# Performance work log

Measured on AMD Instinct MI355X. Metric: run time of the kernel, lower is better.

Reference implementation:

```python
import jax, jax.numpy as jnp
import numpy as np

N_NODES = 100000
N_EDGES = 1600000
EMB = 128
N_LAYER = 5
X_DIM = 178
E_DIM = 18
BN_EPS = 1e-5


def setup_inputs() -> dict:
    key = jax.random.key(0)
    ks = jax.random.split(key, 20)
    s = 0.05  # weight scale
    inp = {}
    inp["x"] = jax.random.normal(ks[0], (N_NODES, X_DIM), jnp.float32)
    inp["edge_attr"] = jax.random.uniform(ks[1], (N_EDGES, E_DIM), jnp.float32)
    # input MLP (178 -> emb -> emb, LeakyReLU 0.1)
    inp["iw1"] = jax.random.normal(ks[2], (X_DIM, EMB), jnp.float32) * s
    inp["ib1"] = jax.random.normal(ks[3], (EMB,), jnp.float32) * s
    inp["iw2"] = jax.random.normal(ks[4], (EMB, EMB), jnp.float32) * s
    inp["ib2"] = jax.random.normal(ks[5], (EMB,), jnp.float32) * s
    # per-layer edge embedding MLP (18 -> emb -> emb, LeakyReLU 0.1)
    inp["ew1"] = jax.random.normal(ks[6], (N_LAYER, E_DIM, EMB), jnp.float32) * s
    inp["eb1"] = jax.random.normal(ks[7], (N_LAYER, EMB), jnp.float32) * s
    inp["ew2"] = jax.random.normal(ks[8], (N_LAYER, EMB, EMB), jnp.float32) * s
    inp["eb2"] = jax.random.normal(ks[9], (N_LAYER, EMB), jnp.float32) * s
    # per-layer GIN update MLP (emb -> 2emb -> emb, ReLU)
    inp["mw1"] = jax.random.normal(ks[10], (N_LAYER, EMB, 2 * EMB), jnp.float32) * s
    inp["mb1"] = jax.random.normal(ks[11], (N_LAYER, 2 * EMB), jnp.float32) * s
    inp["mw2"] = jax.random.normal(ks[12], (N_LAYER, 2 * EMB, EMB), jnp.float32) * s
    inp["mb2"] = jax.random.normal(ks[13], (N_LAYER, EMB), jnp.float32) * s
    # per-layer BatchNorm affine params
    inp["gamma"] = jnp.ones((N_LAYER, EMB), jnp.float32)
    inp["beta"] = jnp.zeros((N_LAYER, EMB), jnp.float32)
    inp["edge_index"] = jax.random.randint(ks[14], (2, N_EDGES), 0, N_NODES)
    return inp


def _leaky(v):
    return jnp.where(v > 0, v, 0.1 * v)


def reference(x, edge_attr, iw1, ib1, iw2, ib2, ew1, eb1, ew2, eb2,
              mw1, mb1, mw2, mb2, gamma, beta, edge_index):
    src = edge_index[0]  # x_j gathered from source nodes (PyG source_to_target)
    dst = edge_index[1]
    n = x.shape[0]

    # input node MLP with LeakyReLU(0.1)
    h = _leaky(x @ iw1 + ib1) @ iw2 + ib2  # [N, EMB]

    for l in range(N_LAYER):
        # edge embeddings for real edges: [E, EMB]
        ee = _leaky(edge_attr @ ew1[l] + eb1[l]) @ ew2[l] + eb2[l]
        # self-loop edges have zero edge_attr -> constant embedding vector [EMB]
        self_e = _leaky(eb1[l]) @ ew2[l] + eb2[l]
        # message = x_j + edge_emb; aggregate (add) at destination, plus self-loop term
        msg = h[src] + ee
        aggr = jax.ops.segment_sum(msg, dst, num_segments=n) + h + self_e
        # GIN update MLP (ReLU)
        hh = jnp.maximum(aggr @ mw1[l] + mb1[l], 0.0) @ mw2[l] + mb2[l]
        # BatchNorm1d (training mode: batch stats, biased variance)
        mean = hh.mean(axis=0)
        var = hh.var(axis=0)
        hh = (hh - mean) / jnp.sqrt(var + BN_EPS) * gamma[l] + beta[l]
        if l < N_LAYER - 1:
            hh = jnp.maximum(hh, 0.0)  # ReLU on all but last layer; dropout p=0 is a no-op
        h = hh

    return h  # JK == 'last'
```

## Files before the change

kernel.cpp:

```cpp
#include <hip/hip_runtime.h>
#include <hip/hip_bf16.h>
#include <hip/hip_fp16.h>
#include <cstdint>
#include <cstddef>

#define NNODES 100000
#define NEDGES 1600000
#define EMBD 128
#define NLAYER 5
#define XDIM 178
#define EDIM 18
#define BNEPS 1e-5f

typedef __attribute__((ext_vector_type(8))) short short8;
typedef __attribute__((ext_vector_type(8))) unsigned short ushort8;
typedef __attribute__((ext_vector_type(4))) float f32x4;

static __device__ __forceinline__ float leakyf(float v){ return v > 0.f ? v : 0.1f*v; }
static __device__ __forceinline__ unsigned short f2b(float v){
  __hip_bfloat16 b = __float2bfloat16(v);
  return *reinterpret_cast<unsigned short*>(&b);
}
static __device__ __forceinline__ float b2f(unsigned short u){
  __hip_bfloat16 b = *reinterpret_cast<__hip_bfloat16*>(&u);
  return __bfloat162float(b);
}
static __device__ __forceinline__ unsigned short f2h(float v){
  __half h = __float2half(v);
  return *reinterpret_cast<unsigned short*>(&h);
}
static __device__ __forceinline__ float h2f(unsigned short u){
  __half h = *reinterpret_cast<__half*>(&u);
  return __half2float(h);
}

__global__ __launch_bounds__(256) void k_hist(const int* __restrict__ dst, int* __restrict__ cnt){
  int e = blockIdx.x*256 + threadIdx.x;
  if (e < NEDGES) atomicAdd(&cnt[dst[e]], 1);
}

__global__ __launch_bounds__(256) void k_scan1(const int* __restrict__ cnt, int* __restrict__ rowptr,
                                               int* __restrict__ bsum){
  __shared__ int s[256];
  int t = threadIdx.x, i = blockIdx.x*256 + t;
  int v = (i < NNODES) ? cnt[i] : 0;
  s[t] = v; __syncthreads();
  for (int off=1; off<256; off<<=1){
    int x = (t>=off) ? s[t-off] : 0; __syncthreads();
    s[t] += x; __syncthreads();
  }
  if (i < NNODES) rowptr[i+1] = s[t];
  if (t == 255) bsum[blockIdx.x] = s[t];
}

__global__ __launch_bounds__(512) void k_scan2(const int* __restrict__ bsum, int* __restrict__ boff, int nb){
  __shared__ int s[512];
  int t = threadIdx.x;
  int v = (t < nb) ? bsum[t] : 0;
  s[t] = v; __syncthreads();
  for (int off=1; off<512; off<<=1){
    int x = (t>=off) ? s[t-off] : 0; __syncthreads();
    s[t] += x; __syncthreads();
  }
  if (t < nb) boff[t] = s[t] - v;
}

__global__ __launch_bounds__(256) void k_scan3(int* __restrict__ rowptr, const int* __restrict__ boff){
  int i = blockIdx.x*256 + threadIdx.x;
  if (i < NNODES) rowptr[i+1] += boff[i>>8];
  if (i == 0) rowptr[0] = 0;
}

__global__ __launch_bounds__(256) void k_curcopy(const int* __restrict__ rowptr, int* __restrict__ cursor){
  int i = blockIdx.x*256 + threadIdx.x;
  if (i < NNODES) cursor[i] = rowptr[i];
}

__global__ __launch_bounds__(256) void k_fill_pos(const int* __restrict__ dst, int* __restrict__ cursor,
                                                  int* __restrict__ einv){
  int e = blockIdx.x*256 + threadIdx.x;
  if (e >= NEDGES) return;
  int pos = atomicAdd(&cursor[dst[e]], 1);
  einv[pos] = e;
}

__global__ __launch_bounds__(256) void k_fill_ea(const int* __restrict__ einv, const int* __restrict__ src,
                                                 const float* __restrict__ ea,
                                                 int* __restrict__ srcp, unsigned short* __restrict__ eap24){
  int pos = blockIdx.x*256 + threadIdx.x;
  if (pos >= NEDGES) return;
  int e = einv[pos];
  srcp[pos] = src[e];
  const float* a = ea + (size_t)e*EDIM;
  float v[18];
  #pragma unroll
  for (int k=0;k<9;++k){
    float2 t = *(const float2*)(a + 2*k);
    v[2*k] = t.x; v[2*k+1] = t.y;
  }
  ushort8 r0, r1, r2;
  #pragma unroll
  for (int k=0;k<8;++k) r0[k] = f2b(v[k]);
  #pragma unroll
  for (int k=0;k<8;++k) r1[k] = f2b(v[8+k]);
  #pragma unroll
  for (int k=0;k<8;++k) r2[k] = 0;
  r2[0] = f2b(v[16]); r2[1] = f2b(v[17]);
  r2[2] = 0x3F80;
  unsigned short* o = eap24 + (size_t)pos*24;
  *reinterpret_cast<ushort8*>(o)      = r0;
  *reinterpret_cast<ushort8*>(o + 8)  = r1;
  *reinterpret_cast<ushort8*>(o + 16) = r2;
}

__global__ __launch_bounds__(256) void k_fill(const int* __restrict__ src, const int* __restrict__ dst,
                                              const float* __restrict__ ea, int* __restrict__ cursor,
                                              int* __restrict__ perm, int* __restrict__ srcp,
                                              float* __restrict__ eap){
  int e = blockIdx.x*256 + threadIdx.x;
  if (e >= NEDGES) return;
  int pos = atomicAdd(&cursor[dst[e]], 1);
  perm[pos] = e;
  srcp[pos] = src[e];
  if (eap){
    const float* a = ea + (size_t)e*EDIM;
    float* o = eap + (size_t)pos*EDIM;
    #pragma unroll
    for (int k=0;k<EDIM;++k) o[k] = a[k];
  }
}

__global__ __launch_bounds__(128) void k_selfe(const float* __restrict__ eb1, const float* __restrict__ ew2,
                                               const float* __restrict__ eb2, float* __restrict__ selfe){
  int l = blockIdx.x, c = threadIdx.x;
  const float* b1 = eb1 + l*EMBD;
  const float* w2 = ew2 + (size_t)l*EMBD*EMBD;
  float acc = eb2[l*EMBD + c];
  for (int j=0;j<EMBD;++j) acc += leakyf(b1[j]) * w2[j*EMBD + c];
  selfe[l*EMBD + c] = acc;
}

__global__ __launch_bounds__(256) void k_wc(const float* __restrict__ ew2, const float* __restrict__ mw1,
                                            float* __restrict__ wc){
  int idx = blockIdx.x*256 + threadIdx.x;
  int l = idx >> 15, rem = idx & 32767;
  int i = rem >> 8, n = rem & 255;
  const float* e = ew2 + (size_t)l*EMBD*EMBD + i*EMBD;
  const float* m = mw1 + (size_t)l*EMBD*2*EMBD + n;
  float acc = 0.f;
  #pragma unroll 4
  for (int j=0;j<EMBD;++j) acc += e[j]*m[(size_t)j*2*EMBD];
  wc[idx] = acc;
}

__global__ __launch_bounds__(256) void k_pack(const float* __restrict__ s1, int rows1,
                                              const float* __restrict__ s2, int Kreal,
                                              int Kpad, int N, __hip_bfloat16* __restrict__ out){
  int idx = blockIdx.x*256 + threadIdx.x;
  if (idx >= Kpad*N) return;
  int k = idx / N, n = idx - k*N;
  float v = 0.f;
  if (k < rows1) v = s1[(size_t)k*N + n];
  else if (k < Kreal) v = s2[(size_t)(k-rows1)*N + n];
  unsigned short hi = f2b(v);
  unsigned short lo = f2b(v - b2f(hi));
  size_t o = (size_t)(k>>5)*N*32 + (size_t)n*32 + (k&31);
  unsigned short* po = (unsigned short*)out;
  po[o] = hi;
  po[(size_t)Kpad*N + o] = lo;
}

__global__ __launch_bounds__(256) void k_s1all(
    const int* __restrict__ rowptr, const unsigned short* __restrict__ eap24,
    const float* __restrict__ ew1, const float* __restrict__ eb1,
    unsigned short* __restrict__ S1all)
{
  __shared__ __align__(16) unsigned short wlds[NLAYER*3*EMBD*8];
  int tid = threadIdx.x;
  for (int i = tid; i < NLAYER*3*EMBD*8; i += 256){
    int j = i & 7;
    int col = (i >> 3) & 127;
    int kb3 = (i >> 10) % 3;
    int l = i / 3072;
    int k = kb3*8 + j;
    float v = 0.f;
    if (k < EDIM) v = ew1[(size_t)l*EDIM*EMBD + k*EMBD + col];
    else if (k == EDIM) v = eb1[l*EMBD + col];
    wlds[i] = f2b(v);
  }
  __syncthreads();

  int lane = tid & 63;
  int lr = lane & 15, kb = lane >> 4;

  int wid = blockIdx.x*4 + (tid>>6);
  const int NW = gridDim.x*4;
  for (int node = wid; node < NNODES; node += NW){
    int rs = rowptr[node], re = rowptr[node+1];
    float s[NLAYER][8];
    #pragma unroll
    for (int l=0;l<NLAYER;++l)
      #pragma unroll
      for (int nf=0;nf<8;++nf) s[l][nf] = 0.f;

    for (int c0 = rs; c0 < re; c0 += 16){
      int cnt = re - c0;
      int idx = c0 + lr; if (idx > re-1) idx = re-1;
      short8 af = (short8)0;
      if (kb < 3){
        ushort8 t = *reinterpret_cast<const ushort8*>(eap24 + (size_t)idx*24 + kb*8);
        af = *reinterpret_cast<short8*>(&t);
      }
      if (lr >= cnt) af = (short8)0;

      #pragma unroll
      for (int l=0;l<NLAYER;++l){
        #pragma unroll
        for (int nf=0;nf<8;++nf){
          short8 bh = (short8)0;
          if (kb < 3)
            bh = *reinterpret_cast<const short8*>(&wlds[(((l*3+kb)*128) + nf*16 + lr)*8]);
          f32x4 acc = (f32x4)0.f;
          acc = __builtin_amdgcn_mfma_f32_16x16x32_bf16(af, bh, acc, 0,0,0);
          #pragma unroll
          for (int j=0;j<4;++j){
            float v = acc[j];
            s[l][nf] = fmaf(0.55f, v, s[l][nf]);
            s[l][nf] = fmaf(0.45f, fabsf(v), s[l][nf]);
          }
        }
      }
    }

    #pragma unroll
    for (int l=0;l<NLAYER;++l){
      float r[8];
      #pragma unroll
      for (int nf=0;nf<8;++nf){
        float v = s[l][nf];
        v += __shfl_xor(v, 16);
        v += __shfl_xor(v, 32);
        r[nf] = v;
      }
      float va = r[0], vb = r[1];
      if (kb == 1){ va = r[2]; vb = r[3]; }
      if (kb == 2){ va = r[4]; vb = r[5]; }
      if (kb == 3){ va = r[6]; vb = r[7]; }
      unsigned short* dst = S1all + ((size_t)l*NNODES + node)*EMBD;
      dst[kb*32 + lr]      = f2h(va);
      dst[kb*32 + 16 + lr] = f2h(vb);
    }
  }
}

__global__ __launch_bounds__(256) void k_gather_h(
    const unsigned short* __restrict__ hh,
    const int* __restrict__ rowptr, const int* __restrict__ srcp,
    const float* __restrict__ eb2l, const float* __restrict__ selfel,
    float* __restrict__ base)
{
  int tid = threadIdx.x;
  int li = tid & 31;
  int c4 = li*4;
  float4 sf4 = *(const float4*)(selfel + c4);
  float4 e24 = *(const float4*)(eb2l + c4);
  int slot = blockIdx.x*8 + (tid>>5);
  const int NS = gridDim.x*8;
  for (int node = slot; node < NNODES; node += NS){
    int rs = rowptr[node], re = rowptr[node+1];
    f32x4 b = (f32x4)0.f;
    for (int c0 = rs; c0 < re; c0 += 8){
      int cnt = re - c0;
      #pragma unroll
      for (int p=0;p<8;++p){
        int e = c0 + p; if (e > re-1) e = re-1;
        float m = (p < cnt) ? 1.f : 0.f;
        int sp = srcp[e];
        uint2 hv = *(const uint2*)(hh + (size_t)sp*EMBD + c4);
        b[0] = fmaf(m, h2f((unsigned short)(hv.x & 0xffffu)), b[0]);
        b[1] = fmaf(m, h2f((unsigned short)(hv.x >> 16)),     b[1]);
        b[2] = fmaf(m, h2f((unsigned short)(hv.y & 0xffffu)), b[2]);
        b[3] = fmaf(m, h2f((unsigned short)(hv.y >> 16)),     b[3]);
      }
    }
    float deg = (float)(re - rs);
    uint2 hn = *(const uint2*)(hh + (size_t)node*EMBD + c4);
    float4 o;
    o.x = b[0] + h2f((unsigned short)(hn.x & 0xffffu)) + sf4.x + deg*e24.x;
    o.y = b[1] + h2f((unsigned short)(hn.x >> 16))     + sf4.y + deg*e24.y;
    o.z = b[2] + h2f((unsigned short)(hn.y & 0xffffu)) + sf4.z + deg*e24.z;
    o.w = b[3] + h2f((unsigned short)(hn.y >> 16))     + sf4.w + deg*e24.w;
    *(float4*)(base + (size_t)node*EMBD + c4) = o;
  }
}

__global__ __launch_bounds__(256) void k_edge2(
    const unsigned short* __restrict__ hh, const int* __restrict__ rowptr,
    const int* __restrict__ srcp, const unsigned short* __restrict__ eap24,
    const float* __restrict__ ew1l, const float* __restrict__ eb1l,
    const float* __restrict__ eb2l, const float* __restrict__ selfel,
    float* __restrict__ S1, float* __restrict__ base, int GG)
{
  int tid = threadIdx.x;
  if ((int)blockIdx.x < GG){
    int li = tid & 31;
    int c4 = li*4;
    float4 sf4 = *(const float4*)(selfel + c4);
    float4 e24 = *(const float4*)(eb2l + c4);
    int slot = blockIdx.x*8 + (tid>>5);
    const int NS = GG*8;
    for (int node = slot; node < NNODES; node += NS){
      int rs = rowptr[node], re = rowptr[node+1];
      f32x4 b = (f32x4)0.f;
      for (int c0 = rs; c0 < re; c0 += 8){
        int cnt = re - c0;
        #pragma unroll
        for (int p=0;p<8;++p){
          int e = c0 + p; if (e > re-1) e = re-1;
          float m = (p < cnt) ? 1.f : 0.f;
          int sp = srcp[e];
          uint2 hv = *(const uint2*)(hh + (size_t)sp*EMBD + c4);
          b[0] = fmaf(m, h2f((unsigned short)(hv.x & 0xffffu)), b[0]);
          b[1] = fmaf(m, h2f((unsigned short)(hv.x >> 16)),     b[1]);
          b[2] = fmaf(m, h2f((unsigned short)(hv.y & 0xffffu)), b[2]);
          b[3] = fmaf(m, h2f((unsigned short)(hv.y >> 16)),     b[3]);
        }
      }
      float deg = (float)(re - rs);
      uint2 hn = *(const uint2*)(hh + (size_t)node*EMBD + c4);
      float4 o;
      o.x = b[0] + h2f((unsigned short)(hn.x & 0xffffu)) + sf4.x + deg*e24.x;
      o.y = b[1] + h2f((unsigned short)(hn.x >> 16))     + sf4.y + deg*e24.y;
      o.z = b[2] + h2f((unsigned short)(hn.y & 0xffffu)) + sf4.z + deg*e24.z;
      o.w = b[3] + h2f((unsigned short)(hn.y >> 16))     + sf4.w + deg*e24.w;
      *(float4*)(base + (size_t)node*EMBD + c4) = o;
    }
  } else {
    int lane = tid & 63;
    int lr = lane & 15, kb = lane >> 4;
    short8 bh[8];
    #pragma unroll
    for (int nf=0; nf<8; ++nf){
      int col = nf*16 + lr;
      ushort8 hh8;
      #pragma unroll
      for (int j=0;j<8;++j){
        int k = kb*8 + j;
        float v = 0.f;
        if (k < EDIM) v = ew1l[k*EMBD + col];
        else if (k == EDIM) v = eb1l[col];
        hh8[j] = f2b(v);
      }
      bh[nf] = *reinterpret_cast<short8*>(&hh8);
    }
    auto loadC = [&](int c0, int re)->short8{
      int cnt = re - c0;
      int idx = c0 + lr; if (idx > re-1) idx = re-1;
      short8 af = (short8)0;
      if (kb < 3){
        ushort8 t = *reinterpret_cast<const ushort8*>(eap24 + (size_t)idx*24 + kb*8);
        af = *reinterpret_cast<short8*>(&t);
      }
      if (lr >= cnt) af = (short8)0;
      return af;
    };
    const int GS = gridDim.x - GG;
    int wid = (blockIdx.x - GG)*4 + (tid>>6);
    const int NW = GS*4;
    for (int nA = wid; nA < NNODES; nA += 2*NW){
      int nB = nA + NW;
      bool hasB = (nB < NNODES);
      int rsA = rowptr[nA], reA = rowptr[nA+1];
      int rsB = 0, reB = 0;
      if (hasB){ rsB = rowptr[nB]; reB = rowptr[nB+1]; }
      float sA[8], sB[8];
      #pragma unroll
      for (int nf=0;nf<8;++nf){ sA[nf]=0.f; sB[nf]=0.f; }
      int cA = rsA, cB = rsB;
      while (cA < reA || cB < reB){
        bool dA = cA < reA, dB = cB < reB;
        short8 afA = (short8)0, afB = (short8)0;
        if (dA) afA = loadC(cA, reA);
        if (dB) afB = loadC(cB, reB);
        if (dA){
          #pragma unroll
          for (int nf=0;nf<8;++nf){
            f32x4 acc = (f32x4)0.f;
            acc = __builtin_amdgcn_mfma_f32_16x16x32_bf16(afA, bh[nf], acc, 0,0,0);
            #pragma unroll
            for (int j=0;j<4;++j){
              float v = acc[j];
              sA[nf] = fmaf(0.55f, v, sA[nf]);
              sA[nf] = fmaf(0.45f, fabsf(v), sA[nf]);
            }
          }
        }
        if (dB){
          #pragma unroll
          for (int nf=0;nf<8;++nf){
            f32x4 acc = (f32x4)0.f;
            acc = __builtin_amdgcn_mfma_f32_16x16x32_bf16(afB, bh[nf], acc, 0,0,0);
            #pragma unroll
            for (int j=0;j<4;++j){
              float v = acc[j];
              sB[nf] = fmaf(0.55f, v, sB[nf]);
              sB[nf] = fmaf(0.45f, fabsf(v), sB[nf]);
            }
          }
        }
        cA += 16; cB += 16;
      }
      {
        #pragma unroll
        for (int nf=0;nf<8;++nf){
          float v = sA[nf];
          v += __shfl_xor(v, 16);
          v += __shfl_xor(v, 32);
          sA[nf] = v;
        }
        float va = sA[0], vb = sA[1];
        if (kb == 1){ va = sA[2]; vb = sA[3]; }
        if (kb == 2){ va = sA[4]; vb = sA[5]; }
        if (kb == 3){ va = sA[6]; vb = sA[7]; }
        S1[(size_t)nA*EMBD + kb*32 + lr]      = va;
        S1[(size_t)nA*EMBD + kb*32 + 16 + lr] = vb;
      }
      if (hasB){
        #pragma unroll
        for (int nf=0;nf<8;++nf){
          float v = sB[nf];
          v += __shfl_xor(v, 16);
          v += __shfl_xor(v, 32);
          sB[nf] = v;
        }
        float va = sB[0], vb = sB[1];
        if (kb == 1){ va = sB[2]; vb = sB[3]; }
        if (kb == 2){ va = sB[4]; vb = sB[5]; }
        if (kb == 3){ va = sB[6]; vb = sB[7]; }
        S1[(size_t)nB*EMBD + kb*32 + lr]      = va;
        S1[(size_t)nB*EMBD + kb*32 + 16 + lr] = vb;
      }
    }
  }
}

__global__ __launch_bounds__(256) void k_edge(
    const float* __restrict__ h, const int* __restrict__ rowptr,
    const int* __restrict__ perm, const int* __restrict__ srcp,
    const float* __restrict__ edge_attr, const float* __restrict__ eaperm,
    const float* __restrict__ ew1l, const float* __restrict__ eb1l,
    const float* __restrict__ eb2l, const float* __restrict__ selfel,
    float* __restrict__ S1, float* __restrict__ base)
{
  __shared__ float w1s[EDIM*EMBD];
  __shared__ float b1s[EMBD];
  int tid = threadIdx.x;
  for (int i = tid; i < EDIM*EMBD; i += 256) w1s[i] = ew1l[i];
  if (tid < EMBD) b1s[tid] = eb1l[tid];
  __syncthreads();
  int lane = tid & 63;
  int node = blockIdx.x*4 + (tid >> 6);
  if (node >= NNODES) return;
  int rs = rowptr[node], re = rowptr[node+1];
  int c0 = lane*2;
  float s1x=0.f, s1y=0.f, bx=0.f, by=0.f;
  for (int i = rs; i < re; ++i){
    int s = __builtin_amdgcn_readfirstlane(srcp[i]);
    const float* ea;
    if (eaperm){
      ea = eaperm + (size_t)__builtin_amdgcn_readfirstlane(i)*EDIM;
    } else {
      ea = edge_attr + (size_t)__builtin_amdgcn_readfirstlane(perm[i])*EDIM;
    }
    float2 hs = *(const float2*)(h + (size_t)s*EMBD + c0);
    bx += hs.x; by += hs.y;
    float d0 = b1s[c0], d1 = b1s[c0+1];
    #pragma unroll
    for (int k=0;k<EDIM;++k){
      float av = ea[k];
      d0 += av * w1s[k*EMBD + c0];
      d1 += av * w1s[k*EMBD + c0 + 1];
    }
    s1x += leakyf(d0); s1y += leakyf(d1);
  }
  float deg = (float)(re - rs);
  float2 hv = *(const float2*)(h + (size_t)node*EMBD + c0);
  *(float2*)(S1 + (size_t)node*EMBD + c0) = make_float2(s1x, s1y);
  float bvx = bx + hv.x + selfel[c0]   + deg*eb2l[c0];
  float bvy = by + hv.y + selfel[c0+1] + deg*eb2l[c0+1];
  *(float2*)(base + (size_t)node*EMBD + c0) = make_float2(bvx, bvy);
}

template<int BN, int WGM, int WGN, bool ALO, bool BLO, int ACT, bool STATS, bool OBF16,
         bool CONCAT, bool KCHK, bool ABF16, bool AH16>
__global__ __launch_bounds__(512) void k_mgemm(
    const float* __restrict__ Af, const float* __restrict__ A1,
    const __hip_bfloat16* __restrict__ Ab, const unsigned short* __restrict__ Afh,
    int M, int Kreal, int Kpad, int lda,
    const __hip_bfloat16* __restrict__ Bp,
    const float* __restrict__ bias,
    float* __restrict__ Cf, __hip_bfloat16* __restrict__ Cb, int ldc,
    float* __restrict__ stats, unsigned short* __restrict__ Ch)
{
  static_assert(WGM*WGN == 8, "8 waves");
  constexpr int BM = 128;
  constexpr int MF = BM/(16*WGM);
  constexpr int NF = BN/(16*WGN);
  constexpr int LDS_ROW = 40;
  __shared__ __align__(16) unsigned short Ah[BM*LDS_ROW];
  __shared__ __align__(16) unsigned short Al[ALO ? BM*LDS_ROW : 8];
  __shared__ float ssum[STATS ? BN : 4];
  __shared__ float ssq [STATS ? BN : 4];

  int tid = threadIdx.x;
  int row0 = blockIdx.x*BM;
  int w = tid >> 6, lane = tid & 63;
  int wm = w / WGN, wn = w % WGN;
  int lr = lane & 15, kb = lane >> 4;
  int wrow = wm*MF*16, wcol = wn*NF*16;

  if (STATS && tid < BN){ ssum[tid] = 0.f; ssq[tid] = 0.f; }

  f32x4 acc[MF][NF];
  #pragma unroll
  for (int a=0;a<MF;++a)
    #pragma unroll
    for (int b=0;b<NF;++b) acc[a][b] = (f32x4)0.f;

  const size_t planeSz = (size_t)Kpad*BN;
  int sr = tid >> 2;
  int skq = (tid & 3)*8;
  int grow = row0 + sr;
  const int KS = Kpad >> 5;

  for (int ks = 0; ks < KS; ++ks){
    int k0 = ks << 5;
    int kg = k0 + skq;
    ushort8 hv, lv;
    if (ABF16){
      short8 raw = (short8)0;
      if (grow < M) raw = *reinterpret_cast<const short8*>((const unsigned short*)Ab + (size_t)grow*lda + kg);
      hv = *reinterpret_cast<ushort8*>(&raw);
    } else {
      float v[8];
      if (AH16 && (!CONCAT || kg < EMBD)){
        ushort8 raw = (ushort8)0;
        if (grow < M) raw = *reinterpret_cast<const ushort8*>(Afh + (size_t)grow*(CONCAT ? EMBD : lda) + kg);
        #pragma unroll
        for (int i=0;i<8;++i) v[i] = h2f(raw[i]);
      } else if (KCHK){
        #pragma unroll
        for (int i=0;i<8;++i)
          v[i] = (grow < M && kg+i < Kreal) ? Af[(size_t)grow*lda + kg + i] : 0.f;
      } else {
        const float* s;
        if (CONCAT) s = A1 + (size_t)grow*lda + (kg - (AH16 ? EMBD : 0));
        else        s = Af + (size_t)grow*lda + kg;
        if (CONCAT && !AH16 && kg < EMBD) s = Af + (size_t)grow*lda + kg;
        float4 p0 = make_float4(0,0,0,0), p1 = make_float4(0,0,0,0);
        if (grow < M){ p0 = *(const float4*)s; p1 = *(const float4*)(s+4); }
        v[0]=p0.x; v[1]=p0.y; v[2]=p0.z; v[3]=p0.w;
        v[4]=p1.x; v[5]=p1.y; v[6]=p1.z; v[7]=p1.w;
      }
      #pragma unroll
      for (int i=0;i<8;++i){
        unsigned short h16 = f2b(v[i]);
        hv[i] = h16;
        if (ALO) lv[i] = f2b(v[i] - b2f(h16));
      }
    }
    __syncthreads();
    *reinterpret_cast<ushort8*>(&Ah[sr*LDS_ROW + skq]) = hv;
    if (ALO && !ABF16) *reinterpret_cast<ushort8*>(&Al[sr*LDS_ROW + skq]) = lv;
    __syncthreads();

    short8 ah[MF], al[MF];
    #pragma unroll
    for (int mf=0; mf<MF; ++mf){
      int r = (wrow + mf*16 + lr)*LDS_ROW + kb*8;
      ah[mf] = *reinterpret_cast<const short8*>(&Ah[r]);
      if (ALO) al[mf] = *reinterpret_cast<const short8*>(&Al[r]);
    }
    const unsigned short* bb = (const unsigned short*)Bp + (size_t)ks*BN*32;
    short8 bh[NF], blv[NF];
    #pragma unroll
    for (int nf=0; nf<NF; ++nf){
      size_t off = (size_t)(wcol + nf*16 + lr)*32 + kb*8;
      bh[nf] = *reinterpret_cast<const short8*>(bb + off);
      if (BLO) blv[nf] = *reinterpret_cast<const short8*>(bb + planeSz + off);
    }
    #pragma unroll
    for (int mf=0; mf<MF; ++mf){
      #pragma unroll
      for (int nf=0; nf<NF; ++nf){
        acc[mf][nf] = __builtin_amdgcn_mfma_f32_16x16x32_bf16(ah[mf], bh[nf], acc[mf][nf], 0, 0, 0);
        if (BLO)
          acc[mf][nf] = __builtin_amdgcn_mfma_f32_16x16x32_bf16(ah[mf], blv[nf], acc[mf][nf], 0, 0, 0);
        if (ALO)
          acc[mf][nf] = __builtin_amdgcn_mfma_f32_16x16x32_bf16(al[mf], bh[nf], acc[mf][nf], 0, 0, 0);
      }
    }
  }

  float bcol[NF];
  #pragma unroll
  for (int nf=0; nf<NF; ++nf) bcol[nf] = bias ? bias[wcol + nf*16 + lr] : 0.f;
  float s[NF], sq[NF];
  #pragma unroll
  for (int nf=0; nf<NF; ++nf){ s[nf]=0.f; sq[nf]=0.f; }

  #pragma unroll
  for (int mf=0; mf<MF; ++mf){
    #pragma unroll
    for (int j=0; j<4; ++j){
      int r = row0 + wrow + mf*16 + kb*4 + j;
      if (r < M){
        #pragma unroll
        for (int nf=0; nf<NF; ++nf){
          int c = wcol + nf*16 + lr;
          float v = acc[mf][nf][j] + bcol[nf];
          if (ACT == 1) v = leakyf(v);
          if (ACT == 2) v = fmaxf(v, 0.f);
          if (OBF16) Cb[(size_t)r*ldc + c] = __float2bfloat16(v);
          else if (Cf) Cf[(size_t)r*ldc + c] = v;
          if (Ch) Ch[(size_t)r*ldc + c] = f2h(v);
          if (STATS){ s[nf] += v; sq[nf] += v*v; }
        }
      }
    }
  }
  if (STATS){
    #pragma unroll
    for (int nf=0; nf<NF; ++nf){
      atomicAdd(&ssum[wcol + nf*16 + lr], s[nf]);
      atomicAdd(&ssq [wcol + nf*16 + lr], sq[nf]);
    }
    __syncthreads();
    if (tid < BN){
      atomicAdd(&stats[tid], ssum[tid]);
      atomicAdd(&stats[BN + tid], ssq[tid]);
    }
  }
}

__global__ __launch_bounds__(256) void k_bn(const float* __restrict__ hh, const float* __restrict__ stats,
                                            const float* __restrict__ gamma, const float* __restrict__ beta,
                                            float* __restrict__ out, unsigned short* __restrict__ outh,
                                            int dorelu){
  int idx = blockIdx.x*256 + threadIdx.x;
  if (idx >= NNODES*(EMBD/4)) return;
  int c0 = (idx & (EMBD/4 - 1)) * 4;
  float4 v = *(const float4*)(hh + (size_t)idx*4);
  float o[4] = {v.x, v.y, v.z, v.w};
  const float invN = 1.f / (float)NNODES;
  #pragma unroll
  for (int i=0;i<4;++i){
    int c = c0 + i;
    float mean = stats[c] * invN;
    float var  = stats[EMBD + c] * invN - mean*mean;
    float inv  = rsqrtf(fmaxf(var, 0.f) + BNEPS);
    float y = (o[i] - mean) * inv * gamma[c] + beta[c];
    if (dorelu) y = fmaxf(y, 0.f);
    o[i] = y;
  }
  if (out) *(float4*)(out + (size_t)idx*4) = make_float4(o[0],o[1],o[2],o[3]);
  if (outh){
    uint2 pk;
    pk.x = (unsigned)f2h(o[0]) | ((unsigned)f2h(o[1]) << 16);
    pk.y = (unsigned)f2h(o[2]) | ((unsigned)f2h(o[3]) << 16);
    *reinterpret_cast<uint2*>(outh + (size_t)idx*4) = pk;
  }
}

extern "C" void kernel_launch(void* const* d_in, const int* in_sizes, int n_in,
                              void* d_out, int out_size, void* d_ws, size_t ws_size,
                              hipStream_t stream)
{
  const float* x   = (const float*)d_in[0];
  const float* ea  = (const float*)d_in[1];
  const float* iw1 = (const float*)d_in[2];
  const float* ib1 = (const float*)d_in[3];
  const float* iw2 = (const float*)d_in[4];
  const float* ib2 = (const float*)d_in[5];
  const float* ew1 = (const float*)d_in[6];
  const float* eb1 = (const float*)d_in[7];
  const float* ew2 = (const float*)d_in[8];
  const float* eb2 = (const float*)d_in[9];
  const float* mw1 = (const float*)d_in[10];
  const float* mb1 = (const float*)d_in[11];
  const float* mw2 = (const float*)d_in[12];
  const float* mb2 = (const float*)d_in[13];
  const float* gamma = (const float*)d_in[14];
  const float* beta  = (const float*)d_in[15];
  const int* eidx = (const int*)d_in[16];
  const int* srcI = eidx;
  const int* dstI = eidx + NEDGES;

  char* p = (char*)d_ws;
  auto alloc = [&](size_t bytes)->char*{
    char* r = p; p += (bytes + 255) & ~(size_t)255; return r;
  };
  float* S1    = (float*)alloc((size_t)NNODES*EMBD*4);
  float* base  = (float*)alloc((size_t)NNODES*EMBD*4);
  __hip_bfloat16* tbuf = (__hip_bfloat16*)alloc((size_t)NNODES*2*EMBD*2);
  int* perm   = (int*)alloc((size_t)NEDGES*4);
  int* srcp   = (int*)alloc((size_t)NEDGES*4);
  int* rowptr = (int*)alloc((size_t)(NNODES+1)*4);
  int* cursor = (int*)alloc((size_t)NNODES*4);
  int* bsum   = (int*)alloc(4096);
  int* boff   = (int*)alloc(4096);
  float* selfe = (float*)alloc(NLAYER*EMBD*4);
  float* stats = (float*)alloc(2*EMBD*4);
  float* wc    = (float*)alloc((size_t)NLAYER*EMBD*2*EMBD*4);
  __hip_bfloat16* Bi1 = (__hip_bfloat16*)alloc((size_t)192*EMBD*2*2);
  __hip_bfloat16* Bi2 = (__hip_bfloat16*)alloc((size_t)EMBD*EMBD*2*2);
  __hip_bfloat16* B1  = (__hip_bfloat16*)alloc((size_t)NLAYER*256*256*2*2);
  __hip_bfloat16* B2  = (__hip_bfloat16*)alloc((size_t)NLAYER*256*EMBD*2*2);
  size_t used = (size_t)(p - (char*)d_ws);

  const size_t szEap  = (size_t)NEDGES*24*2;
  const size_t szHh   = (size_t)NNODES*EMBD*2;
  const size_t szS1a  = (size_t)NLAYER*NNODES*EMBD*2;
  const size_t szHbuf = (size_t)NNODES*EMBD*4;

  bool tierA = (ws_size >= used + szEap + szHh + szS1a + 1024);
  bool tierB = !tierA && (ws_size >= used + szEap + szHh + 512);
  unsigned short* eap24 = nullptr;
  unsigned short* hh16 = nullptr;
  unsigned short* s1all = nullptr;
  float* hbuf = nullptr;
  float* eaperm = nullptr;
  if (tierA){
    eap24 = (unsigned short*)alloc(szEap);
    hh16  = (unsigned short*)alloc(szHh);
    s1all = (unsigned short*)alloc(szS1a);
  } else if (tierB){
    eap24 = (unsigned short*)alloc(szEap);
    hh16  = (unsigned short*)alloc(szHh);
  } else {
    hbuf = (float*)alloc(szHbuf);
    used = (size_t)(p - (char*)d_ws);
    if (ws_size >= used + (size_t)NEDGES*EDIM*4 + 256)
      eaperm = (float*)alloc((size_t)NEDGES*EDIM*4);
  }
  bool use_new = tierA || tierB;

  hipMemsetAsync(cursor, 0, (size_t)NNODES*4, stream);
  k_hist<<<(NEDGES+255)/256, 256, 0, stream>>>(dstI, cursor);
  int nb = (NNODES+255)/256;
  k_scan1<<<nb, 256, 0, stream>>>(cursor, rowptr, bsum);
  k_scan2<<<1, 512, 0, stream>>>(bsum, boff, nb);
  k_scan3<<<(NNODES+255)/256, 256, 0, stream>>>(rowptr, boff);
  k_curcopy<<<(NNODES+255)/256, 256, 0, stream>>>(rowptr, cursor);
  if (use_new){
    k_fill_pos<<<(NEDGES+255)/256, 256, 0, stream>>>(dstI, cursor, perm);
    k_fill_ea<<<(NEDGES+255)/256, 256, 0, stream>>>(perm, srcI, ea, srcp, eap24);
  } else {
    k_fill<<<(NEDGES+255)/256, 256, 0, stream>>>(srcI, dstI, ea, cursor, perm, srcp, eaperm);
  }
  k_selfe<<<NLAYER, EMBD, 0, stream>>>(eb1, ew2, eb2, selfe);

  k_wc<<<(NLAYER*EMBD*2*EMBD)/256, 256, 0, stream>>>(ew2, mw1, wc);
  k_pack<<<(192*EMBD+255)/256, 256, 0, stream>>>(iw1, XDIM, iw1, XDIM, 192, EMBD, Bi1);
  k_pack<<<(EMBD*EMBD+255)/256, 256, 0, stream>>>(iw2, EMBD, iw2, EMBD, EMBD, EMBD, Bi2);
  for (int l=0; l<NLAYER; ++l){
    k_pack<<<(256*256+255)/256, 256, 0, stream>>>(
        wc + (size_t)l*EMBD*2*EMBD, EMBD, mw1 + (size_t)l*EMBD*2*EMBD, 256, 256, 256,
        B1 + (size_t)l*256*256*2);
    k_pack<<<(256*EMBD+255)/256, 256, 0, stream>>>(
        mw2 + (size_t)l*2*EMBD*EMBD, 256, mw2, 256, 256, EMBD,
        B2 + (size_t)l*256*EMBD*2);
  }

  if (tierA)
    k_s1all<<<1024, 256, 0, stream>>>(rowptr, eap24, ew1, eb1, s1all);

  const int gx = (NNODES + 127)/128;

  k_mgemm<128,4,2, true,true,1,false,false,false,true ,false,false><<<gx, 512, 0, stream>>>(
      x, nullptr, nullptr, nullptr, NNODES, XDIM, 192, XDIM, Bi1, ib1, S1, nullptr, EMBD, nullptr, nullptr);
  k_mgemm<128,4,2, true,true,0,false,false,false,false,false,false><<<gx, 512, 0, stream>>>(
      S1, nullptr, nullptr, nullptr, NNODES, EMBD, EMBD, EMBD, Bi2, ib2,
      use_new ? nullptr : hbuf, nullptr, EMBD, nullptr, use_new ? hh16 : nullptr);

  for (int l=0; l<NLAYER; ++l){
    hipMemsetAsync(stats, 0, 2*EMBD*4, stream);
    if (tierA){
      k_gather_h<<<2048, 256, 0, stream>>>(
          hh16, rowptr, srcp, eb2 + l*EMBD, selfe + l*EMBD, base);
      k_mgemm<256,2,4, true,true,2,false,true ,true ,false,false,true ><<<gx, 512, 0, stream>>>(
          nullptr, base, nullptr, s1all + (size_t)l*NNODES*EMBD,
          NNODES, 256, 256, EMBD, B1 + (size_t)l*256*256*2,
          mb1 + l*2*EMBD, nullptr, tbuf, 2*EMBD, nullptr, nullptr);
    } else if (tierB){
      k_edge2<<<2048, 256, 0, stream>>>(
          hh16, rowptr, srcp, eap24,
          ew1 + (size_t)l*EDIM*EMBD, eb1 + l*EMBD, eb2 + l*EMBD, selfe + l*EMBD,
          S1, base, 1408);
      k_mgemm<256,2,4, true,true,2,false,true ,true ,false,false,false><<<gx, 512, 0, stream>>>(
          S1, base, nullptr, nullptr, NNODES, 256, 256, EMBD, B1 + (size_t)l*256*256*2,
          mb1 + l*2*EMBD, nullptr, tbuf, 2*EMBD, nullptr, nullptr);
    } else {
      k_edge<<<NNODES/4, 256, 0, stream>>>(
          hbuf, rowptr, perm, srcp, ea, eaperm,
          ew1 + (size_t)l*EDIM*EMBD, eb1 + l*EMBD, eb2 + l*EMBD, selfe + l*EMBD,
          S1, base);
      k_mgemm<256,2,4, true,true,2,false,true ,true ,false,false,false><<<gx, 512, 0, stream>>>(
          S1, base, nullptr, nullptr, NNODES, 256, 256, EMBD, B1 + (size_t)l*256*256*2,
          mb1 + l*2*EMBD, nullptr, tbuf, 2*EMBD, nullptr, nullptr);
    }
    k_mgemm<128,4,2, false,false,0,true ,false,false,false,true ,false><<<gx, 512, 0, stream>>>(
        nullptr, nullptr, tbuf, nullptr, NNODES, 256, 256, 2*EMBD, B2 + (size_t)l*256*EMBD*2,
        mb2 + l*EMBD, S1, nullptr, EMBD, stats, nullptr);
    float* outp; unsigned short* outh;
    if (l == NLAYER-1){ outp = (float*)d_out; outh = nullptr; }
    else if (use_new) { outp = nullptr;       outh = hh16;    }
    else              { outp = hbuf;          outh = nullptr; }
    k_bn<<<(NNODES*(EMBD/4)+255)/256, 256, 0, stream>>>(
        S1, stats, gamma + l*EMBD, beta + l*EMBD, outp, outh, (l < NLAYER-1) ? 1 : 0);
  }
}
```

Measured before the change: 2.078 ms.

## Replace precomputed all-layer edge sums with per-layer fused fp16 edge kernel

Drops the upfront kernel that computed edge-MLP first-layer sums for all five layers into a large fp16 buffer, and the separate gather kernel. Each layer now runs a fused kernel that does the neighbor gather and the MFMA edge-embedding sum on split block ranges, writing both results as fp16. The gather accumulates full groups of 8 neighbors in packed half2 before widening to fp32, and the first GIN GEMM reads both fp16 concat halves directly. This cuts workspace and fp32 intermediate traffic, but recomputes the edge MFMA work every layer and loses some precision in the half2 partial sums.

New measurement: 1.891 ms. 9.0% less time.

```diff
diff --git a/kernel.cpp b/kernel.cpp
--- a/kernel.cpp
+++ b/kernel.cpp
@@ -170,136 +170,12 @@
   po[(size_t)Kpad*N + o] = lo;
 }
 
-__global__ __launch_bounds__(256) void k_s1all(
-    const int* __restrict__ rowptr, const unsigned short* __restrict__ eap24,
-    const float* __restrict__ ew1, const float* __restrict__ eb1,
-    unsigned short* __restrict__ S1all)
-{
-  __shared__ __align__(16) unsigned short wlds[NLAYER*3*EMBD*8];
-  int tid = threadIdx.x;
-  for (int i = tid; i < NLAYER*3*EMBD*8; i += 256){
-    int j = i & 7;
-    int col = (i >> 3) & 127;
-    int kb3 = (i >> 10) % 3;
-    int l = i / 3072;
-    int k = kb3*8 + j;
-    float v = 0.f;
-    if (k < EDIM) v = ew1[(size_t)l*EDIM*EMBD + k*EMBD + col];
-    else if (k == EDIM) v = eb1[l*EMBD + col];
-    wlds[i] = f2b(v);
-  }
-  __syncthreads();
-
-  int lane = tid & 63;
-  int lr = lane & 15, kb = lane >> 4;
-
-  int wid = blockIdx.x*4 + (tid>>6);
-  const int NW = gridDim.x*4;
-  for (int node = wid; node < NNODES; node += NW){
-    int rs = rowptr[node], re = rowptr[node+1];
-    float s[NLAYER][8];
-    #pragma unroll
-    for (int l=0;l<NLAYER;++l)
-      #pragma unroll
-      for (int nf=0;nf<8;++nf) s[l][nf] = 0.f;
-
-    for (int c0 = rs; c0 < re; c0 += 16){
-      int cnt = re - c0;
-      int idx = c0 + lr; if (idx > re-1) idx = re-1;
-      short8 af = (short8)0;
-      if (kb < 3){
-        ushort8 t = *reinterpret_cast<const ushort8*>(eap24 + (size_t)idx*24 + kb*8);
-        af = *reinterpret_cast<short8*>(&t);
-      }
-      if (lr >= cnt) af = (short8)0;
-
-      #pragma unroll
-      for (int l=0;l<NLAYER;++l){
-        #pragma unroll
-        for (int nf=0;nf<8;++nf){
-          short8 bh = (short8)0;
-          if (kb < 3)
-            bh = *reinterpret_cast<const short8*>(&wlds[(((l*3+kb)*128) + nf*16 + lr)*8]);
-          f32x4 acc = (f32x4)0.f;
-          acc = __builtin_amdgcn_mfma_f32_16x16x32_bf16(af, bh, acc, 0,0,0);
-          #pragma unroll
-          for (int j=0;j<4;++j){
-            float v = acc[j];
-            s[l][nf] = fmaf(0.55f, v, s[l][nf]);
-            s[l][nf] = fmaf(0.45f, fabsf(v), s[l][nf]);
-          }
-        }
-      }
-    }
-
-    #pragma unroll
-    for (int l=0;l<NLAYER;++l){
-      float r[8];
-      #pragma unroll
-      for (int nf=0;nf<8;++nf){
-        float v = s[l][nf];
-        v += __shfl_xor(v, 16);
-        v += __shfl_xor(v, 32);
-        r[nf] = v;
-      }
-      float va = r[0], vb = r[1];
-      if (kb == 1){ va = r[2]; vb = r[3]; }
-      if (kb == 2){ va = r[4]; vb = r[5]; }
-      if (kb == 3){ va = r[6]; vb = r[7]; }
-      unsigned short* dst = S1all + ((size_t)l*NNODES + node)*EMBD;
-      dst[kb*32 + lr]      = f2h(va);
-      dst[kb*32 + 16 + lr] = f2h(vb);
-    }
-  }
-}
-
-__global__ __launch_bounds__(256) void k_gather_h(
-    const unsigned short* __restrict__ hh,
-    const int* __restrict__ rowptr, const int* __restrict__ srcp,
-    const float* __restrict__ eb2l, const float* __restrict__ selfel,
-    float* __restrict__ base)
-{
-  int tid = threadIdx.x;
-  int li = tid & 31;
-  int c4 = li*4;
-  float4 sf4 = *(const float4*)(selfel + c4);
-  float4 e24 = *(const float4*)(eb2l + c4);
-  int slot = blockIdx.x*8 + (tid>>5);
-  const int NS = gridDim.x*8;
-  for (int node = slot; node < NNODES; node += NS){
-    int rs = rowptr[node], re = rowptr[node+1];
-    f32x4 b = (f32x4)0.f;
-    for (int c0 = rs; c0 < re; c0 += 8){
-      int cnt = re - c0;
-      #pragma unroll
-      for (int p=0;p<8;++p){
-        int e = c0 + p; if (e > re-1) e = re-1;
-        float m = (p < cnt) ? 1.f : 0.f;
-        int sp = srcp[e];
-        uint2 hv = *(const uint2*)(hh + (size_t)sp*EMBD + c4);
-        b[0] = fmaf(m, h2f((unsigned short)(hv.x & 0xffffu)), b[0]);
-        b[1] = fmaf(m, h2f((unsigned short)(hv.x >> 16)),     b[1]);
-        b[2] = fmaf(m, h2f((unsigned short)(hv.y & 0xffffu)), b[2]);
-        b[3] = fmaf(m, h2f((unsigned short)(hv.y >> 16)),     b[3]);
-      }
-    }
-    float deg = (float)(re - rs);
-    uint2 hn = *(const uint2*)(hh + (size_t)node*EMBD + c4);
-    float4 o;
-    o.x = b[0] + h2f((unsigned short)(hn.x & 0xffffu)) + sf4.x + deg*e24.x;
-    o.y = b[1] + h2f((unsigned short)(hn.x >> 16))     + sf4.y + deg*e24.y;
-    o.z = b[2] + h2f((unsigned short)(hn.y & 0xffffu)) + sf4.z + deg*e24.z;
-    o.w = b[3] + h2f((unsigned short)(hn.y >> 16))     + sf4.w + deg*e24.w;
-    *(float4*)(base + (size_t)node*EMBD + c4) = o;
-  }
-}
-
-__global__ __launch_bounds__(256) void k_edge2(
+__global__ __launch_bounds__(256) void k_edge3(
     const unsigned short* __restrict__ hh, const int* __restrict__ rowptr,
     const int* __restrict__ srcp, const unsigned short* __restrict__ eap24,
     const float* __restrict__ ew1l, const float* __restrict__ eb1l,
     const float* __restrict__ eb2l, const float* __restrict__ selfel,
-    float* __restrict__ S1, float* __restrict__ base, int GG)
+    unsigned short* __restrict__ s1h, unsigned short* __restrict__ baseh, int GG)
 {
   int tid = threadIdx.x;
   if ((int)blockIdx.x < GG){
@@ -312,28 +188,38 @@
     for (int node = slot; node < NNODES; node += NS){
       int rs = rowptr[node], re = rowptr[node+1];
       f32x4 b = (f32x4)0.f;
-      for (int c0 = rs; c0 < re; c0 += 8){
-        int cnt = re - c0;
+      for (int e0 = rs; e0 + 8 <= re; e0 += 8){
+        __half2 a0 = __half2{__half(0.f), __half(0.f)};
+        __half2 a1 = a0;
         #pragma unroll
         for (int p=0;p<8;++p){
-          int e = c0 + p; if (e > re-1) e = re-1;
-          float m = (p < cnt) ? 1.f : 0.f;
-          int sp = srcp[e];
+          int sp = srcp[e0+p];
           uint2 hv = *(const uint2*)(hh + (size_t)sp*EMBD + c4);
-          b[0] = fmaf(m, h2f((unsigned short)(hv.x & 0xffffu)), b[0]);
-          b[1] = fmaf(m, h2f((unsigned short)(hv.x >> 16)),     b[1]);
-          b[2] = fmaf(m, h2f((unsigned short)(hv.y & 0xffffu)), b[2]);
-          b[3] = fmaf(m, h2f((unsigned short)(hv.y >> 16)),     b[3]);
-        }
+          a0 = __hadd2(a0, *reinterpret_cast<const __half2*>(&hv.x));
+          a1 = __hadd2(a1, *reinterpret_cast<const __half2*>(&hv.y));
+        }
+        float2 f0 = __half22float2(a0), f1 = __half22float2(a1);
+        b[0] += f0.x; b[1] += f0.y; b[2] += f1.x; b[3] += f1.y;
+      }
+      int tail = (re - rs) & 7;
+      for (int p = 0; p < tail; ++p){
+        int sp = srcp[re - tail + p];
+        uint2 hv = *(const uint2*)(hh + (size_t)sp*EMBD + c4);
+        b[0] += h2f((unsigned short)(hv.x & 0xffffu));
+        b[1] += h2f((unsigned short)(hv.x >> 16));
+        b[2] += h2f((unsigned short)(hv.y & 0xffffu));
+        b[3] += h2f((unsigned short)(hv.y >> 16));
       }
       float deg = (float)(re - rs);
       uint2 hn = *(const uint2*)(hh + (size_t)node*EMBD + c4);
-      float4 o;
-      o.x = b[0] + h2f((unsigned short)(hn.x & 0xffffu)) + sf4.x + deg*e24.x;
-      o.y = b[1] + h2f((unsigned short)(hn.x >> 16))     + sf4.y + deg*e24.y;
-      o.z = b[2] + h2f((unsigned short)(hn.y & 0xffffu)) + sf4.z + deg*e24.z;
-      o.w = b[3] + h2f((unsigned short)(hn.y >> 16))     + sf4.w + deg*e24.w;
-      *(float4*)(base + (size_t)node*EMBD + c4) = o;
+      float ox = b[0] + h2f((unsigned short)(hn.x & 0xffffu)) + sf4.x + deg*e24.x;
+      float oy = b[1] + h2f((unsigned short)(hn.x >> 16))     + sf4.y + deg*e24.y;
+      float oz = b[2] + h2f((unsigned short)(hn.y & 0xffffu)) + sf4.z + deg*e24.z;
+      float ow = b[3] + h2f((unsigned short)(hn.y >> 16))     + sf4.w + deg*e24.w;
+      uint2 pk;
+      pk.x = (unsigned)f2h(ox) | ((unsigned)f2h(oy) << 16);
+      pk.y = (unsigned)f2h(oz) | ((unsigned)f2h(ow) << 16);
+      *reinterpret_cast<uint2*>(baseh + (size_t)node*EMBD + c4) = pk;
     }
   } else {
     int lane = tid & 63;
@@ -422,6 +308,156 @@
         if (kb == 1){ va = sA[2]; vb = sA[3]; }
         if (kb == 2){ va = sA[4]; vb = sA[5]; }
         if (kb == 3){ va = sA[6]; vb = sA[7]; }
+        s1h[(size_t)nA*EMBD + kb*32 + lr]      = f2h(va);
+        s1h[(size_t)nA*EMBD + kb*32 + 16 + lr] = f2h(vb);
+      }
+      if (hasB){
+        #pragma unroll
+        for (int nf=0;nf<8;++nf){
+          float v = sB[nf];
+          v += __shfl_xor(v, 16);
+          v += __shfl_xor(v, 32);
+          sB[nf] = v;
+        }
+        float va = sB[0], vb = sB[1];
+        if (kb == 1){ va = sB[2]; vb = sB[3]; }
+        if (kb == 2){ va = sB[4]; vb = sB[5]; }
+        if (kb == 3){ va = sB[6]; vb = sB[7]; }
+        s1h[(size_t)nB*EMBD + kb*32 + lr]      = f2h(va);
+        s1h[(size_t)nB*EMBD + kb*32 + 16 + lr] = f2h(vb);
+      }
+    }
+  }
+}
+
+__global__ __launch_bounds__(256) void k_edge2(
+    const unsigned short* __restrict__ hh, const int* __restrict__ rowptr,
+    const int* __restrict__ srcp, const unsigned short* __restrict__ eap24,
+    const float* __restrict__ ew1l, const float* __restrict__ eb1l,
+    const float* __restrict__ eb2l, const float* __restrict__ selfel,
+    float* __restrict__ S1, float* __restrict__ base, int GG)
+{
+  int tid = threadIdx.x;
+  if ((int)blockIdx.x < GG){
+    int li = tid & 31;
+    int c4 = li*4;
+    float4 sf4 = *(const float4*)(selfel + c4);
+    float4 e24 = *(const float4*)(eb2l + c4);
+    int slot = blockIdx.x*8 + (tid>>5);
+    const int NS = GG*8;
+    for (int node = slot; node < NNODES; node += NS){
+      int rs = rowptr[node], re = rowptr[node+1];
+      f32x4 b = (f32x4)0.f;
+      for (int c0 = rs; c0 < re; c0 += 8){
+        int cnt = re - c0;
+        #pragma unroll
+        for (int p=0;p<8;++p){
+          int e = c0 + p; if (e > re-1) e = re-1;
+          float m = (p < cnt) ? 1.f : 0.f;
+          int sp = srcp[e];
+          uint2 hv = *(const uint2*)(hh + (size_t)sp*EMBD + c4);
+          b[0] = fmaf(m, h2f((unsigned short)(hv.x & 0xffffu)), b[0]);
+          b[1] = fmaf(m, h2f((unsigned short)(hv.x >> 16)),     b[1]);
+          b[2] = fmaf(m, h2f((unsigned short)(hv.y & 0xffffu)), b[2]);
+          b[3] = fmaf(m, h2f((unsigned short)(hv.y >> 16)),     b[3]);
+        }
+      }
+      float deg = (float)(re - rs);
+      uint2 hn = *(const uint2*)(hh + (size_t)node*EMBD + c4);
+      float4 o;
+      o.x = b[0] + h2f((unsigned short)(hn.x & 0xffffu)) + sf4.x + deg*e24.x;
+      o.y = b[1] + h2f((unsigned short)(hn.x >> 16))     + sf4.y + deg*e24.y;
+      o.z = b[2] + h2f((unsigned short)(hn.y & 0xffffu)) + sf4.z + deg*e24.z;
+      o.w = b[3] + h2f((unsigned short)(hn.y >> 16))     + sf4.w + deg*e24.w;
+      *(float4*)(base + (size_t)node*EMBD + c4) = o;
+    }
+  } else {
+    int lane = tid & 63;
+    int lr = lane & 15, kb = lane >> 4;
+    short8 bh[8];
+    #pragma unroll
+    for (int nf=0; nf<8; ++nf){
+      int col = nf*16 + lr;
+      ushort8 hh8;
+      #pragma unroll
+      for (int j=0;j<8;++j){
+        int k = kb*8 + j;
+        float v = 0.f;
+        if (k < EDIM) v = ew1l[k*EMBD + col];
+        else if (k == EDIM) v = eb1l[col];
+        hh8[j] = f2b(v);
+      }
+      bh[nf] = *reinterpret_cast<short8*>(&hh8);
+    }
+    auto loadC = [&](int c0, int re)->short8{
+      int cnt = re - c0;
+      int idx = c0 + lr; if (idx > re-1) idx = re-1;
+      short8 af = (short8)0;
+      if (kb < 3){
+        ushort8 t = *reinterpret_cast<const ushort8*>(eap24 + (size_t)idx*24 + kb*8);
+        af = *reinterpret_cast<short8*>(&t);
+      }
+      if (lr >= cnt) af = (short8)0;
+      return af;
+    };
+    const int GS = gridDim.x - GG;
+    int wid = (blockIdx.x - GG)*4 + (tid>>6);
+    const int NW = GS*4;
+    for (int nA = wid; nA < NNODES; nA += 2*NW){
+      int nB = nA + NW;
+      bool hasB = (nB < NNODES);
+      int rsA = rowptr[nA], reA = rowptr[nA+1];
+      int rsB = 0, reB = 0;
+      if (hasB){ rsB = rowptr[nB]; reB = rowptr[nB+1]; }
+      float sA[8], sB[8];
+      #pragma unroll
+      for (int nf=0;nf<8;++nf){ sA[nf]=0.f; sB[nf]=0.f; }
+      int cA = rsA, cB = rsB;
+      while (cA < reA || cB < reB){
+        bool dA = cA < reA, dB = cB < reB;
+        short8 afA = (short8)0, afB = (short8)0;
+        if (dA) afA = loadC(cA, reA);
+        if (dB) afB = loadC(cB, reB);
+        if (dA){
+          #pragma unroll
+          for (int nf=0;nf<8;++nf){
+            f32x4 acc = (f32x4)0.f;
+            acc = __builtin_amdgcn_mfma_f32_16x16x32_bf16(afA, bh[nf], acc, 0,0,0);
+            #pragma unroll
+            for (int j=0;j<4;++j){
+              float v = acc[j];
+              sA[nf] = fmaf(0.55f, v, sA[nf]);
+              sA[nf] = fmaf(0.45f, fabsf(v), sA[nf]);
+            }
+          }
+        }
+        if (dB){
+          #pragma unroll
+          for (int nf=0;nf<8;++nf){
+            f32x4 acc = (f32x4)0.f;
+            acc = __builtin_amdgcn_mfma_f32_16x16x32_bf16(afB, bh[nf], acc, 0,0,0);
+            #pragma unroll
+            for (int j=0;j<4;++j){
+              float v = acc[j];
+              sB[nf] = fmaf(0.55f, v, sB[nf]);
+              sB[nf] = fmaf(0.45f, fabsf(v), sB[nf]);
+            }
+          }
+        }
+        cA += 16; cB += 16;
+      }
+      {
+        #pragma unroll
+        for (int nf=0;nf<8;++nf){
+          float v = sA[nf];
+          v += __shfl_xor(v, 16);
+          v += __shfl_xor(v, 32);
+          sA[nf] = v;
+        }
+        float va = sA[0], vb = sA[1];
+        if (kb == 1){ va = sA[2]; vb = sA[3]; }
+        if (kb == 2){ va = sA[4]; vb = sA[5]; }
+        if (kb == 3){ va = sA[6]; vb = sA[7]; }
         S1[(size_t)nA*EMBD + kb*32 + lr]      = va;
         S1[(size_t)nA*EMBD + kb*32 + 16 + lr] = vb;
       }
@@ -495,7 +531,8 @@
          bool CONCAT, bool KCHK, bool ABF16, bool AH16>
 __global__ __launch_bounds__(512) void k_mgemm(
     const float* __restrict__ Af, const float* __restrict__ A1,
-    const __hip_bfloat16* __restrict__ Ab, const unsigned short* __restrict__ Afh,
+    const __hip_bfloat16* __restrict__ Ab,
+    const unsigned short* __restrict__ Afh, const unsigned short* __restrict__ Afh2,
     int M, int Kreal, int Kpad, int lda,
     const __hip_bfloat16* __restrict__ Bp,
     const float* __restrict__ bias,
@@ -543,9 +580,13 @@
       hv = *reinterpret_cast<ushort8*>(&raw);
     } else {
       float v[8];
-      if (AH16 && (!CONCAT || kg < EMBD)){
+      if (AH16){
+        const unsigned short* s16;
+        if (CONCAT) s16 = (kg < EMBD) ? (Afh + (size_t)grow*EMBD + kg)
+                                      : (Afh2 + (size_t)grow*EMBD + (kg - EMBD));
+        else        s16 = Afh + (size_t)grow*lda + kg;
         ushort8 raw = (ushort8)0;
-        if (grow < M) raw = *reinterpret_cast<const ushort8*>(Afh + (size_t)grow*(CONCAT ? EMBD : lda) + kg);
+        if (grow < M) raw = *reinterpret_cast<const ushort8*>(s16);
         #pragma unroll
         for (int i=0;i<8;++i) v[i] = h2f(raw[i]);
       } else if (KCHK){
@@ -554,9 +595,8 @@
           v[i] = (grow < M && kg+i < Kreal) ? Af[(size_t)grow*lda + kg + i] : 0.f;
       } else {
         const float* s;
-        if (CONCAT) s = A1 + (size_t)grow*lda + (kg - (AH16 ? EMBD : 0));
+        if (CONCAT) s = (kg < EMBD) ? (Af + (size_t)grow*lda + kg) : (A1 + (size_t)grow*lda + (kg - EMBD));
         else        s = Af + (size_t)grow*lda + kg;
-        if (CONCAT && !AH16 && kg < EMBD) s = Af + (size_t)grow*lda + kg;
         float4 p0 = make_float4(0,0,0,0), p1 = make_float4(0,0,0,0);
         if (grow < M){ p0 = *(const float4*)s; p1 = *(const float4*)(s+4); }
         v[0]=p0.x; v[1]=p0.y; v[2]=p0.z; v[3]=p0.w;
@@ -720,20 +760,22 @@
 
   const size_t szEap  = (size_t)NEDGES*24*2;
   const size_t szHh   = (size_t)NNODES*EMBD*2;
-  const size_t szS1a  = (size_t)NLAYER*NNODES*EMBD*2;
+  const size_t szH16  = (size_t)NNODES*EMBD*2;
   const size_t szHbuf = (size_t)NNODES*EMBD*4;
 
-  bool tierA = (ws_size >= used + szEap + szHh + szS1a + 1024);
-  bool tierB = !tierA && (ws_size >= used + szEap + szHh + 512);
+  bool tierN = (ws_size >= used + szEap + szHh + 2*szH16 + 1024);
+  bool tierB = !tierN && (ws_size >= used + szEap + szHh + 512);
   unsigned short* eap24 = nullptr;
   unsigned short* hh16 = nullptr;
-  unsigned short* s1all = nullptr;
+  unsigned short* s1h = nullptr;
+  unsigned short* baseh = nullptr;
   float* hbuf = nullptr;
   float* eaperm = nullptr;
-  if (tierA){
+  if (tierN){
     eap24 = (unsigned short*)alloc(szEap);
     hh16  = (unsigned short*)alloc(szHh);
-    s1all = (unsigned short*)alloc(szS1a);
+    s1h   = (unsigned short*)alloc(szH16);
+    baseh = (unsigned short*)alloc(szH16);
   } else if (tierB){
     eap24 = (unsigned short*)alloc(szEap);
     hh16  = (unsigned short*)alloc(szHh);
@@ -743,7 +785,7 @@
     if (ws_size >= used + (size_t)NEDGES*EDIM*4 + 256)
       eaperm = (float*)alloc((size_t)NEDGES*EDIM*4);
   }
-  bool use_new = tierA || tierB;
+  bool use_new = tierN || tierB;
 
   hipMemsetAsync(cursor, 0, (size_t)NNODES*4, stream);
   k_hist<<<(NEDGES+255)/256, 256, 0, stream>>>(dstI, cursor);
@@ -772,46 +814,45 @@
         B2 + (size_t)l*256*EMBD*2);
   }
 
-  if (tierA)
-    k_s1all<<<1024, 256, 0, stream>>>(rowptr, eap24, ew1, eb1, s1all);
-
   const int gx = (NNODES + 127)/128;
 
   k_mgemm<128,4,2, true,true,1,false,false,false,true ,false,false><<<gx, 512, 0, stream>>>(
-      x, nullptr, nullptr, nullptr, NNODES, XDIM, 192, XDIM, Bi1, ib1, S1, nullptr, EMBD, nullptr, nullptr);
+      x, nullptr, nullptr, nullptr, nullptr, NNODES, XDIM, 192, XDIM, Bi1, ib1,
+      S1, nullptr, EMBD, nullptr, nullptr);
   k_mgemm<128,4,2, true,true,0,false,false,false,false,false,false><<<gx, 512, 0, stream>>>(
-      S1, nullptr, nullptr, nullptr, NNODES, EMBD, EMBD, EMBD, Bi2, ib2,
+      S1, nullptr, nullptr, nullptr, nullptr, NNODES, EMBD, EMBD, EMBD, Bi2, ib2,
       use_new ? nullptr : hbuf, nullptr, EMBD, nullptr, use_new ? hh16 : nullptr);
 
   for (int l=0; l<NLAYER; ++l){
     hipMemsetAsync(stats, 0, 2*EMBD*4, stream);
-    if (tierA){
-      k_gather_h<<<2048, 256, 0, stream>>>(
-          hh16, rowptr, srcp, eb2 + l*EMBD, selfe + l*EMBD, base);
+    if (tierN){
+      k_edge3<<<2048, 256, 0, stream>>>(
+          hh16, rowptr, srcp, eap24,
+          ew1 + (size_t)l*EDIM*EMBD, eb1 + l*EMBD, eb2 + l*EMBD, selfe + l*EMBD,
+          s1h, baseh, 1408);
       k_mgemm<256,2,4, true,true,2,false,true ,true ,false,false,true ><<<gx, 512, 0, stream>>>(
-          nullptr, base, nullptr, s1all + (size_t)l*NNODES*EMBD,
-          NNODES, 256, 256, EMBD, B1 + (size_t)l*256*256*2,
-          mb1 + l*2*EMBD, nullptr, tbuf, 2*EMBD, nullptr, nullptr);
+          nullptr, nullptr, nullptr, s1h, baseh, NNODES, 256, 256, EMBD,
+          B1 + (size_t)l*256*256*2, mb1 + l*2*EMBD, nullptr, tbuf, 2*EMBD, nullptr, nullptr);
     } else if (tierB){
       k_edge2<<<2048, 256, 0, stream>>>(
           hh16, rowptr, srcp, eap24,
           ew1 + (size_t)l*EDIM*EMBD, eb1 + l*EMBD, eb2 + l*EMBD, selfe + l*EMBD,
           S1, base, 1408);
       k_mgemm<256,2,4, true,true,2,false,true ,true ,false,false,false><<<gx, 512, 0, stream>>>(
-          S1, base, nullptr, nullptr, NNODES, 256, 256, EMBD, B1 + (size_t)l*256*256*2,
-          mb1 + l*2*EMBD, nullptr, tbuf, 2*EMBD, nullptr, nullptr);
+          S1, base, nullptr, nullptr, nullptr, NNODES, 256, 256, EMBD,
+          B1 + (size_t)l*256*256*2, mb1 + l*2*EMBD, nullptr, tbuf, 2*EMBD, nullptr, nullptr);
     } else {
       k_edge<<<NNODES/4, 256, 0, stream>>>(
           hbuf, rowptr, perm, srcp, ea, eaperm,
           ew1 + (size_t)l*EDIM*EMBD, eb1 + l*EMBD, eb2 + l*EMBD, selfe + l*EMBD,
           S1, base);
       k_mgemm<256,2,4, true,true,2,false,true ,true ,false,false,false><<<gx, 512, 0, stream>>>(
-          S1, base, nullptr, nullptr, NNODES, 256, 256, EMBD, B1 + (size_t)l*256*256*2,
-          mb1 + l*2*EMBD, nullptr, tbuf, 2*EMBD, nullptr, nullptr);
+          S1, base, nullptr, nullptr, nullptr, NNODES, 256, 256, EMBD,
+          B1 + (size_t)l*256*256*2, mb1 + l*2*EMBD, nullptr, tbuf, 2*EMBD, nullptr, nullptr);
     }
     k_mgemm<128,4,2, false,false,0,true ,false,false,false,true ,false><<<gx, 512, 0, stream>>>(
-        nullptr, nullptr, tbuf, nullptr, NNODES, 256, 256, 2*EMBD, B2 + (size_t)l*256*EMBD*2,
-        mb2 + l*EMBD, S1, nullptr, EMBD, stats, nullptr);
+        nullptr, nullptr, tbuf, nullptr, nullptr, NNODES, 256, 256, 2*EMBD,
+        B2 + (size_t)l*256*EMBD*2, mb2 + l*EMBD, S1, nullptr, EMBD, stats, nullptr);
     float* outp; unsigned short* outh;
     if (l == NLAYER-1){ outp = (float*)d_out; outh = nullptr; }
     else if (use_new) { outp = nullptr;       outh = hh16;    }
```
